# Performance work log

Measured on AMD Instinct MI355X. Metric: run time of the kernel, lower is better.

The kernel has to match this reference:

```python
import jax, jax.numpy as jnp
import numpy as np

NUM_SRC = 100000
NUM_DST = 50000
E = 1200000
IN_FEATS = 128
H = 4
D = 16


def setup_inputs() -> dict:
    key = jax.random.key(0)
    ks = jax.random.split(key, 8)
    feat = jax.random.normal(ks[0], (NUM_DST + NUM_SRC, IN_FEATS), dtype=jnp.float32)
    edge_src = jax.random.randint(ks[1], (E,), 0, NUM_SRC)
    edge_dst = jax.random.randint(ks[2], (E,), 0, NUM_DST)
    # parameters (xavier-normal-ish scale)
    W = jax.random.normal(ks[3], (H * D, IN_FEATS), dtype=jnp.float32) * (2.0 / np.sqrt(IN_FEATS + H * D))
    attn_l = jax.random.normal(ks[4], (H, D), dtype=jnp.float32) * (2.0 / np.sqrt(1 + D))
    attn_r = jax.random.normal(ks[5], (H, D), dtype=jnp.float32) * (2.0 / np.sqrt(1 + D))
    bias = jnp.zeros((H * D,), dtype=jnp.float32)
    return {"feat": feat, "W": W, "attn_l": attn_l, "attn_r": attn_r,
            "bias": bias, "edge_src": edge_src, "edge_dst": edge_dst, "num_dst": NUM_DST}


def reference(feat, W, attn_l, attn_r, bias, edge_src, edge_dst, num_dst):
    negative_slope = 0.2
    n_heads, d_out = attn_l.shape
    # fc: [N, in] @ [in, H*D] -> [N, H, D]
    proj = (feat @ W.T).reshape(feat.shape[0], n_heads, d_out)
    feat_dst = proj[:num_dst]      # [num_dst, H, D]
    feat_src = proj[num_dst:]      # [num_src, H, D]
    el = jnp.einsum('nhd,hd->nh', feat_src, attn_l)  # [num_src, H]
    er = jnp.einsum('nhd,hd->nh', feat_dst, attn_r)  # [num_dst, H]
    # per-edge attention logits (u_add_v + leaky_relu)
    e = jax.nn.leaky_relu(el[edge_src] + er[edge_dst], negative_slope)  # [E, H]
    # segment softmax over destination neighborhoods
    m = jax.ops.segment_max(e, edge_dst, num_segments=num_dst)  # [num_dst, H]
    m = jnp.where(jnp.isfinite(m), m, 0.0)
    e_exp = jnp.exp(e - m[edge_dst])
    denom = jax.ops.segment_sum(e_exp, edge_dst, num_segments=num_dst)  # [num_dst, H]
    a = e_exp / denom[edge_dst]  # [E, H]
    # u_mul_e + sum scatter-aggregate
    msg = feat_src[edge_src] * a[:, :, None]  # [E, H, D]
    rst = jax.ops.segment_sum(msg, edge_dst, num_segments=num_dst)  # [num_dst, H, D]
    rst = rst + bias.reshape(1, n_heads, d_out)
    return rst
```

## Files before the change

### kernel.cpp

```cpp
#include <hip/hip_runtime.h>
#include <hip/hip_bf16.h>


#define NEG_SLOPE 0.2f
#define BSHIFT 7
#define BMASK  127
#define MAXBUK 512
#define FSH    12
#define FCAP   4096
#define EB     2048
#define TILES  4

typedef __attribute__((ext_vector_type(8))) short bf16x8;
typedef __attribute__((ext_vector_type(4))) float f32x4;

__device__ __forceinline__ short f2bf(float f) {
    unsigned u = __float_as_uint(f);
    unsigned r = (u + 0x7fffu + ((u >> 16) & 1u)) >> 16;
    return (short)r;
}
__device__ __forceinline__ unsigned pk2(float a, float b) {
    return (unsigned)(unsigned short)f2bf(a) | ((unsigned)(unsigned short)f2bf(b) << 16);
}

__global__ __launch_bounds__(256) void k_init(const float* __restrict__ W,
                                              short* __restrict__ Wb, int nW,
                                              int* __restrict__ bukcnt) {
    for (int i = threadIdx.x; i < nW; i += 256) Wb[i] = f2bf(W[i]);
    for (int i = threadIdx.x; i < MAXBUK; i += 256) bukcnt[i] = 0;
}

__global__ __launch_bounds__(256) void k_proj_bin(
        const float* __restrict__ feat, const short* __restrict__ Wb,
        const float* __restrict__ attn_l, const float* __restrict__ attn_r,
        unsigned short* __restrict__ projb, float* __restrict__ el, float* __restrict__ er,
        int num_tot, int num_dst, int binB,
        const int* __restrict__ es, const int* __restrict__ ed,
        int* __restrict__ bukcnt, unsigned* __restrict__ pairs, int E, int nbuk) {
    __shared__ __align__(16) char smem_[33792];
    if ((int)blockIdx.x >= binB) {
        unsigned short* fs = (unsigned short*)smem_;
        float* fsf = (float*)(smem_ + 16384);
        const int tid = threadIdx.x;
        const int pb = (int)blockIdx.x - binB;

        const int lane = tid & 63;
        const int wv = tid >> 6;
        const int lr = lane & 15;
        const int lg = lane >> 4;

        float4 pf[8];
        int st_row[4], st_col[4];
#pragma unroll
        for (int it = 0; it < 4; it++) {
            int flat = it * 2048 + tid * 8;
            st_row[it] = flat >> 7;
            st_col[it] = flat & 127;
        }

        auto issue = [&](int t) {
            int nb = pb * (TILES * 64) + t * 64;
#pragma unroll
            for (int it = 0; it < 4; it++) {
                int grow = nb + st_row[it];
                if (grow >= num_tot) grow = num_tot - 1;
                const float4* src = (const float4*)(feat + (size_t)grow * 128 + st_col[it]);
                pf[it * 2] = src[0];
                pf[it * 2 + 1] = src[1];
            }
        };
        auto commit = [&]() {
#pragma unroll
            for (int it = 0; it < 4; it++) {
                float4 x = pf[it * 2], y = pf[it * 2 + 1];
                bf16x8 t;
                t[0] = f2bf(x.x); t[1] = f2bf(x.y); t[2] = f2bf(x.z); t[3] = f2bf(x.w);
                t[4] = f2bf(y.x); t[5] = f2bf(y.y); t[6] = f2bf(y.z); t[7] = f2bf(y.w);
                int slot = st_col[it] >> 3;
                int row = st_row[it];
                *(bf16x8*)&fs[row * 128 + ((slot ^ (row & 15)) << 3)] = t;
            }
        };

        issue(0);
        commit();

        for (int t = 0; t < TILES; t++) {
            __syncthreads();

            bf16x8 afrag[4];
#pragma unroll
            for (int c = 0; c < 4; c++)
                afrag[c] = *(const bf16x8*)&fs[(wv * 16 + lr) * 128 + (((c * 4 + lg) ^ lr) << 3)];

            if (t + 1 < TILES) issue(t + 1);

            f32x4 acc[4];
#pragma unroll
            for (int hh = 0; hh < 4; hh++) acc[hh] = f32x4{0.f, 0.f, 0.f, 0.f};
#pragma unroll
            for (int hh = 0; hh < 4; hh++) {
                const short* bp = Wb + (hh * 16 + lr) * 128 + lg * 8;
#pragma unroll
                for (int c = 0; c < 4; c++) {
                    bf16x8 b = *(const bf16x8*)(bp + c * 32);
                    acc[hh] = __builtin_amdgcn_mfma_f32_16x16x32_bf16(afrag[c], b, acc[hh], 0, 0, 0);
                }
            }

#pragma unroll
            for (int hh = 0; hh < 4; hh++)
#pragma unroll
                for (int r = 0; r < 4; r++)
                    fsf[(wv * 16 + lg * 4 + r) * 68 + hh * 16 + lr] = acc[hh][r];
            __syncthreads();

            {
                int row = tid >> 2, seg = tid & 3;
                int n = pb * (TILES * 64) + t * 64 + row;
                if (n < num_tot) {
                    const float4* rp = (const float4*)&fsf[row * 68 + seg * 16];
                    float4 v0 = rp[0], v1 = rp[1], v2 = rp[2], v3 = rp[3];
                    bool is_dst = n < num_dst;
                    const float* attn = is_dst ? attn_r : attn_l;
                    const float4* ap = (const float4*)&attn[seg * 16];
                    float4 a0 = ap[0], a1 = ap[1], a2 = ap[2], a3 = ap[3];
                    float e = v0.x * a0.x + v0.y * a0.y + v0.z * a0.z + v0.w * a0.w
                            + v1.x * a1.x + v1.y * a1.y + v1.z * a1.z + v1.w * a1.w
                            + v2.x * a2.x + v2.y * a2.y + v2.z * a2.z + v2.w * a2.w
                            + v3.x * a3.x + v3.y * a3.y + v3.z * a3.z + v3.w * a3.w;
                    if (is_dst) {
                        er[(size_t)n * 4 + seg] = e;
                    } else {
                        int sN = n - num_dst;
                        el[(size_t)sN * 4 + seg] = e;
                        uint4 q0, q1;
                        q0.x = pk2(v0.x, v0.y); q0.y = pk2(v0.z, v0.w);
                        q0.z = pk2(v1.x, v1.y); q0.w = pk2(v1.z, v1.w);
                        q1.x = pk2(v2.x, v2.y); q1.y = pk2(v2.z, v2.w);
                        q1.z = pk2(v3.x, v3.y); q1.w = pk2(v3.z, v3.w);
                        uint4* dst = (uint4*)(projb + (size_t)sN * 64 + seg * 16);
                        dst[0] = q0; dst[1] = q1;
                    }
                }
            }

            if (t + 1 < TILES) commit();
        }
    } else {
        int* h = (int*)smem_;
        int* cur = (int*)(smem_ + 2048);
        const int tid = threadIdx.x;
        for (int i = tid; i < MAXBUK; i += 256) h[i] = 0;
        __syncthreads();
        int base = (int)blockIdx.x * EB;
        int rd[8], rs[8];
        if (base + EB <= E) {
            const int4* edp = (const int4*)(ed + base + tid * 8);
            const int4* esp = (const int4*)(es + base + tid * 8);
            int4 d0 = edp[0], d1 = edp[1];
            int4 s0 = esp[0], s1 = esp[1];
            rd[0] = d0.x; rd[1] = d0.y; rd[2] = d0.z; rd[3] = d0.w;
            rd[4] = d1.x; rd[5] = d1.y; rd[6] = d1.z; rd[7] = d1.w;
            rs[0] = s0.x; rs[1] = s0.y; rs[2] = s0.z; rs[3] = s0.w;
            rs[4] = s1.x; rs[5] = s1.y; rs[6] = s1.z; rs[7] = s1.w;
#pragma unroll
            for (int i = 0; i < 8; i++) atomicAdd(&h[rd[i] >> BSHIFT], 1);
        } else {
#pragma unroll
            for (int i = 0; i < 8; i++) {
                int idx = base + tid * 8 + i;
                if (idx < E) {
                    rd[i] = ed[idx];
                    rs[i] = es[idx];
                    atomicAdd(&h[rd[i] >> BSHIFT], 1);
                } else {
                    rd[i] = -1;
                }
            }
        }
        __syncthreads();
        for (int i = tid; i < nbuk; i += 256)
            cur[i] = h[i] ? ((i << FSH) + atomicAdd(&bukcnt[i], h[i])) : 0;
        __syncthreads();
#pragma unroll
        for (int i = 0; i < 8; i++) {
            if (rd[i] >= 0) {
                int d = rd[i];
                int bk = d >> BSHIFT;
                int pos = atomicAdd(&cur[bk], 1);
                if (pos < ((bk + 1) << FSH))
                    pairs[pos] = (unsigned)rs[i] | ((unsigned)(d & BMASK) << 25);
            }
        }
    }
}

__global__ __launch_bounds__(256) void k_fillb(unsigned* __restrict__ pairs,
                                               const int* __restrict__ bukcnt,
                                               int* __restrict__ offs,
                                               int* __restrict__ counts, int nd) {
    __shared__ unsigned lp[FCAP];
    __shared__ int h[128], ex[128], cur[128];
    int b = blockIdx.x;
    int s = b << FSH;
    int cnt = bukcnt[b];
    if (cnt > FCAP) cnt = FCAP;
    if (threadIdx.x < 128) h[threadIdx.x] = 0;
    __syncthreads();
    for (int i = threadIdx.x; i < cnt; i += 256) {
        unsigned v = pairs[s + i];
        lp[i] = v;
        atomicAdd(&h[v >> 25], 1);
    }
    __syncthreads();
    if (threadIdx.x < 128) ex[threadIdx.x] = h[threadIdx.x];
    __syncthreads();
    for (int off = 1; off < 128; off <<= 1) {
        int v = (threadIdx.x >= off && threadIdx.x < 128) ? ex[threadIdx.x - off] : 0;
        __syncthreads();
        if (threadIdx.x < 128) ex[threadIdx.x] += v;
        __syncthreads();
    }
    if (threadIdx.x < 128) {
        int e = ex[threadIdx.x] - h[threadIdx.x];
        cur[threadIdx.x] = e;
        int d = (b << BSHIFT) + threadIdx.x;
        if (d < nd) { offs[d] = s + e; counts[d] = h[threadIdx.x]; }
    }
    __syncthreads();
    for (int i = threadIdx.x; i < cnt; i += 256) {
        unsigned v = lp[i];
        int r = atomicAdd(&cur[v >> 25], 1);
        pairs[s + r] = v & 0x1FFFFFFu;
    }
}

__global__ __launch_bounds__(256) void k_agg(
        const unsigned* __restrict__ csr_src, const int* __restrict__ offs,
        const int* __restrict__ counts, const float* __restrict__ el,
        const float* __restrict__ er, const unsigned short* __restrict__ projb,
        const float* __restrict__ bias, float* __restrict__ out, int nd) {
    int wave = (blockIdx.x * 256 + threadIdx.x) >> 6;
    int lane = threadIdx.x & 63;
    if (wave >= nd) return;
    int d = wave;
    int j = lane & 15, h = lane >> 4;
    int q = lane >> 4, cq = lane & 15;
    int hsrc = (cq >> 2) << 4;
    int start = offs[d], deg = counts[d];
    float er_h = er[d * 4 + h];

    float den = 0.f, a0 = 0.f, a1 = 0.f, a2 = 0.f, a3 = 0.f;
    for (int base = 0; base < deg; base += 16) {
        int cend = deg - base;
        if (cend > 16) cend = 16;
        int sidx = 0;
        float w = 0.f;
        if (j < cend) {
            sidx = (int)csr_src[start + base + j];
            float t = el[sidx * 4 + h] + er_h;
            t = t > 0.f ? t : NEG_SLOPE * t;
            w = __expf(fminf(t, 60.f));
        }
        den += w;
        if (cend == 16) {
#pragma unroll
            for (int t4 = 0; t4 < 4; t4++) {
                int e = 4 * t4 + q;
                int s2 = __shfl(sidx, e);
                float w2 = __shfl(w, hsrc | e);
                uint2 pv = *(const uint2*)(projb + (size_t)s2 * 64 + cq * 4);
                a0 += w2 * __uint_as_float(pv.x << 16);
                a1 += w2 * __uint_as_float(pv.x & 0xffff0000u);
                a2 += w2 * __uint_as_float(pv.y << 16);
                a3 += w2 * __uint_as_float(pv.y & 0xffff0000u);
            }
        } else {
            int steps = (cend + 3) >> 2;
            for (int t4 = 0; t4 < steps; t4++) {
                int e = 4 * t4 + q;
                int s2 = __shfl(sidx, e & 15);
                float w2 = __shfl(w, hsrc | (e & 15));
                uint2 pv = *(const uint2*)(projb + (size_t)s2 * 64 + cq * 4);
                a0 += w2 * __uint_as_float(pv.x << 16);
                a1 += w2 * __uint_as_float(pv.x & 0xffff0000u);
                a2 += w2 * __uint_as_float(pv.y << 16);
                a3 += w2 * __uint_as_float(pv.y & 0xffff0000u);
            }
        }
    }

    den += __shfl_xor(den, 1);
    den += __shfl_xor(den, 2);
    den += __shfl_xor(den, 4);
    den += __shfl_xor(den, 8);
    float den_h = __shfl(den, hsrc);

    a0 += __shfl_xor(a0, 16); a0 += __shfl_xor(a0, 32);
    a1 += __shfl_xor(a1, 16); a1 += __shfl_xor(a1, 32);
    a2 += __shfl_xor(a2, 16); a2 += __shfl_xor(a2, 32);
    a3 += __shfl_xor(a3, 16); a3 += __shfl_xor(a3, 32);

    if (q == 0) {
        float rden = den_h > 0.f ? 1.f / den_h : 0.f;
        float4 o;
        o.x = a0 * rden + bias[cq * 4];
        o.y = a1 * rden + bias[cq * 4 + 1];
        o.z = a2 * rden + bias[cq * 4 + 2];
        o.w = a3 * rden + bias[cq * 4 + 3];
        *(float4*)&out[(size_t)d * 64 + cq * 4] = o;
    }
}

extern "C" void kernel_launch(void* const* d_in, const int* in_sizes, int n_in,
                              void* d_out, int out_size, void* d_ws, size_t ws_size,
                              hipStream_t stream) {
    const float* feat   = (const float*)d_in[0];
    const float* W      = (const float*)d_in[1];
    const float* attn_l = (const float*)d_in[2];
    const float* attn_r = (const float*)d_in[3];
    const float* bias   = (const float*)d_in[4];
    const int*   es     = (const int*)d_in[5];
    const int*   ed     = (const int*)d_in[6];

    const int HD      = in_sizes[2];
    const int in_f    = in_sizes[1] / HD;
    const int num_dst = out_size / HD;
    const int num_tot = in_sizes[0] / in_f;
    const int num_src = num_tot - num_dst;
    const int E       = in_sizes[5];

    float* out = (float*)d_out;

    const int NBUK = (num_dst + BMASK) >> BSHIFT;

    unsigned short* projb = (unsigned short*)d_ws;
    float*    el       = (float*)(projb + (size_t)num_src * 64);
    float*    er       = el + (size_t)num_src * 4;
    int*      counts   = (int*)(er + (size_t)num_dst * 4);
    int*      offs     = counts + num_dst;
    int*      bukcnt   = offs + num_dst;
    unsigned* pairs    = (unsigned*)(bukcnt + MAXBUK);
    short*    Wb       = (short*)(pairs + ((size_t)NBUK << FSH));

    const int projB = (num_tot + TILES * 64 - 1) / (TILES * 64);
    const int binB  = (E + EB - 1) / EB;

    k_init<<<1, 256, 0, stream>>>(W, Wb, HD * in_f, bukcnt);

    k_proj_bin<<<binB + projB, 256, 0, stream>>>(
        feat, Wb, attn_l, attn_r, projb, el, er, num_tot, num_dst, binB,
        es, ed, bukcnt, pairs, E, NBUK);

    k_fillb<<<NBUK, 256, 0, stream>>>(pairs, bukcnt, offs, counts, num_dst);

    k_agg<<<(num_dst * 64 + 255) / 256, 256, 0, stream>>>(
        pairs, offs, counts, el, er, projb, bias, out, num_dst);
}
```

Measured before the change: 102.3 us.

## Fuse bucket CSR fill and attention aggregation into one kernel using LDS

Merges the per-bucket counting sort and the per-destination softmax aggregation into a single 1024-thread kernel per bucket. The sorted source indices stay in shared memory instead of being written back to global memory with offs/counts and re-read. This removes a launch and global traffic, but leaves only one block per bucket (a few hundred blocks of 16 waves each), which reduces parallelism and serializes the sort before aggregation in each block.

```diff
diff --git a/kernel.cpp b/kernel.cpp
--- a/kernel.cpp
+++ b/kernel.cpp
@@ -196,120 +196,124 @@
     }
 }
 
-__global__ __launch_bounds__(256) void k_fillb(unsigned* __restrict__ pairs,
-                                               const int* __restrict__ bukcnt,
-                                               int* __restrict__ offs,
-                                               int* __restrict__ counts, int nd) {
-    __shared__ unsigned lp[FCAP];
+__global__ __launch_bounds__(1024) void k_fagg(
+        const unsigned* __restrict__ pairs, const int* __restrict__ bukcnt,
+        const float* __restrict__ el, const float* __restrict__ er,
+        const unsigned short* __restrict__ projb, const float* __restrict__ bias,
+        float* __restrict__ out, int nd) {
+    __shared__ unsigned lpr[FCAP];
+    __shared__ unsigned lps[FCAP];
     __shared__ int h[128], ex[128], cur[128];
-    int b = blockIdx.x;
-    int s = b << FSH;
+    __shared__ float er_s[128 * 4];
+    const int tid = threadIdx.x;
+    const int b = blockIdx.x;
+    const int dbase = b << BSHIFT;
     int cnt = bukcnt[b];
     if (cnt > FCAP) cnt = FCAP;
-    if (threadIdx.x < 128) h[threadIdx.x] = 0;
-    __syncthreads();
-    for (int i = threadIdx.x; i < cnt; i += 256) {
+    const size_t s = (size_t)b << FSH;
+
+    if (tid < 128) h[tid] = 0;
+    if (tid < 512) {
+        int d = dbase + (tid >> 2);
+        er_s[tid] = (d < nd) ? er[(size_t)d * 4 + (tid & 3)] : 0.f;
+    }
+    __syncthreads();
+    for (int i = tid; i < cnt; i += 1024) {
         unsigned v = pairs[s + i];
-        lp[i] = v;
+        lpr[i] = v;
         atomicAdd(&h[v >> 25], 1);
     }
     __syncthreads();
-    if (threadIdx.x < 128) ex[threadIdx.x] = h[threadIdx.x];
+    if (tid < 128) ex[tid] = h[tid];
     __syncthreads();
     for (int off = 1; off < 128; off <<= 1) {
-        int v = (threadIdx.x >= off && threadIdx.x < 128) ? ex[threadIdx.x - off] : 0;
-        __syncthreads();
-        if (threadIdx.x < 128) ex[threadIdx.x] += v;
-        __syncthreads();
-    }
-    if (threadIdx.x < 128) {
-        int e = ex[threadIdx.x] - h[threadIdx.x];
-        cur[threadIdx.x] = e;
-        int d = (b << BSHIFT) + threadIdx.x;
-        if (d < nd) { offs[d] = s + e; counts[d] = h[threadIdx.x]; }
-    }
-    __syncthreads();
-    for (int i = threadIdx.x; i < cnt; i += 256) {
-        unsigned v = lp[i];
+        int v = (tid >= off && tid < 128) ? ex[tid - off] : 0;
+        __syncthreads();
+        if (tid < 128) ex[tid] += v;
+        __syncthreads();
+    }
+    if (tid < 128) cur[tid] = ex[tid] - h[tid];
+    __syncthreads();
+    for (int i = tid; i < cnt; i += 1024) {
+        unsigned v = lpr[i];
         int r = atomicAdd(&cur[v >> 25], 1);
-        pairs[s + r] = v & 0x1FFFFFFu;
-    }
-}
-
-__global__ __launch_bounds__(256) void k_agg(
-        const unsigned* __restrict__ csr_src, const int* __restrict__ offs,
-        const int* __restrict__ counts, const float* __restrict__ el,
-        const float* __restrict__ er, const unsigned short* __restrict__ projb,
-        const float* __restrict__ bias, float* __restrict__ out, int nd) {
-    int wave = (blockIdx.x * 256 + threadIdx.x) >> 6;
-    int lane = threadIdx.x & 63;
-    if (wave >= nd) return;
-    int d = wave;
-    int j = lane & 15, h = lane >> 4;
+        lps[r] = v & 0x1FFFFFFu;
+    }
+    __syncthreads();
+
+    const int lane = tid & 63;
+    const int wid = tid >> 6;
+    int j = lane & 15, hh = lane >> 4;
     int q = lane >> 4, cq = lane & 15;
     int hsrc = (cq >> 2) << 4;
-    int start = offs[d], deg = counts[d];
-    float er_h = er[d * 4 + h];
-
-    float den = 0.f, a0 = 0.f, a1 = 0.f, a2 = 0.f, a3 = 0.f;
-    for (int base = 0; base < deg; base += 16) {
-        int cend = deg - base;
-        if (cend > 16) cend = 16;
-        int sidx = 0;
-        float w = 0.f;
-        if (j < cend) {
-            sidx = (int)csr_src[start + base + j];
-            float t = el[sidx * 4 + h] + er_h;
-            t = t > 0.f ? t : NEG_SLOPE * t;
-            w = __expf(fminf(t, 60.f));
-        }
-        den += w;
-        if (cend == 16) {
-#pragma unroll
-            for (int t4 = 0; t4 < 4; t4++) {
-                int e = 4 * t4 + q;
-                int s2 = __shfl(sidx, e);
-                float w2 = __shfl(w, hsrc | e);
-                uint2 pv = *(const uint2*)(projb + (size_t)s2 * 64 + cq * 4);
-                a0 += w2 * __uint_as_float(pv.x << 16);
-                a1 += w2 * __uint_as_float(pv.x & 0xffff0000u);
-                a2 += w2 * __uint_as_float(pv.y << 16);
-                a3 += w2 * __uint_as_float(pv.y & 0xffff0000u);
-            }
-        } else {
-            int steps = (cend + 3) >> 2;
-            for (int t4 = 0; t4 < steps; t4++) {
-                int e = 4 * t4 + q;
-                int s2 = __shfl(sidx, e & 15);
-                float w2 = __shfl(w, hsrc | (e & 15));
-                uint2 pv = *(const uint2*)(projb + (size_t)s2 * 64 + cq * 4);
-                a0 += w2 * __uint_as_float(pv.x << 16);
-                a1 += w2 * __uint_as_float(pv.x & 0xffff0000u);
-                a2 += w2 * __uint_as_float(pv.y << 16);
-                a3 += w2 * __uint_as_float(pv.y & 0xffff0000u);
-            }
-        }
-    }
-
-    den += __shfl_xor(den, 1);
-    den += __shfl_xor(den, 2);
-    den += __shfl_xor(den, 4);
-    den += __shfl_xor(den, 8);
-    float den_h = __shfl(den, hsrc);
-
-    a0 += __shfl_xor(a0, 16); a0 += __shfl_xor(a0, 32);
-    a1 += __shfl_xor(a1, 16); a1 += __shfl_xor(a1, 32);
-    a2 += __shfl_xor(a2, 16); a2 += __shfl_xor(a2, 32);
-    a3 += __shfl_xor(a3, 16); a3 += __shfl_xor(a3, 32);
-
-    if (q == 0) {
-        float rden = den_h > 0.f ? 1.f / den_h : 0.f;
-        float4 o;
-        o.x = a0 * rden + bias[cq * 4];
-        o.y = a1 * rden + bias[cq * 4 + 1];
-        o.z = a2 * rden + bias[cq * 4 + 2];
-        o.w = a3 * rden + bias[cq * 4 + 3];
-        *(float4*)&out[(size_t)d * 64 + cq * 4] = o;
+
+    for (int dl = wid; dl < 128; dl += 16) {
+        int d = dbase + dl;
+        if (d >= nd) break;
+        int deg = h[dl];
+        int start = ex[dl] - deg;
+        float er_h = er_s[dl * 4 + hh];
+
+        float den = 0.f, a0 = 0.f, a1 = 0.f, a2 = 0.f, a3 = 0.f;
+        for (int base = 0; base < deg; base += 16) {
+            int cend = deg - base;
+            if (cend > 16) cend = 16;
+            int sidx = 0;
+            float w = 0.f;
+            if (j < cend) {
+                sidx = (int)lps[start + base + j];
+                float t = el[sidx * 4 + hh] + er_h;
+                t = t > 0.f ? t : NEG_SLOPE * t;
+                w = __expf(fminf(t, 60.f));
+            }
+            den += w;
+            if (cend == 16) {
+#pragma unroll
+                for (int t4 = 0; t4 < 4; t4++) {
+                    int e = 4 * t4 + q;
+                    int s2 = __shfl(sidx, e);
+                    float w2 = __shfl(w, hsrc | e);
+                    uint2 pv = *(const uint2*)(projb + (size_t)s2 * 64 + cq * 4);
+                    a0 += w2 * __uint_as_float(pv.x << 16);
+                    a1 += w2 * __uint_as_float(pv.x & 0xffff0000u);
+                    a2 += w2 * __uint_as_float(pv.y << 16);
+                    a3 += w2 * __uint_as_float(pv.y & 0xffff0000u);
+                }
+            } else {
+                int steps = (cend + 3) >> 2;
+                for (int t4 = 0; t4 < steps; t4++) {
+                    int e = 4 * t4 + q;
+                    int s2 = __shfl(sidx, e & 15);
+                    float w2 = __shfl(w, hsrc | (e & 15));
+                    uint2 pv = *(const uint2*)(projb + (size_t)s2 * 64 + cq * 4);
+                    a0 += w2 * __uint_as_float(pv.x << 16);
+                    a1 += w2 * __uint_as_float(pv.x & 0xffff0000u);
+                    a2 += w2 * __uint_as_float(pv.y << 16);
+                    a3 += w2 * __uint_as_float(pv.y & 0xffff0000u);
+                }
+            }
+        }
+
+        den += __shfl_xor(den, 1);
+        den += __shfl_xor(den, 2);
+        den += __shfl_xor(den, 4);
+        den += __shfl_xor(den, 8);
+        float den_h = __shfl(den, hsrc);
+
+        a0 += __shfl_xor(a0, 16); a0 += __shfl_xor(a0, 32);
+        a1 += __shfl_xor(a1, 16); a1 += __shfl_xor(a1, 32);
+        a2 += __shfl_xor(a2, 16); a2 += __shfl_xor(a2, 32);
+        a3 += __shfl_xor(a3, 16); a3 += __shfl_xor(a3, 32);
+
+        if (q == 0) {
+            float rden = den_h > 0.f ? 1.f / den_h : 0.f;
+            float4 o;
+            o.x = a0 * rden + bias[cq * 4];
+            o.y = a1 * rden + bias[cq * 4 + 1];
+            o.z = a2 * rden + bias[cq * 4 + 2];
+            o.w = a3 * rden + bias[cq * 4 + 3];
+            *(float4*)&out[(size_t)d * 64 + cq * 4] = o;
+        }
     }
 }
 
@@ -338,9 +342,7 @@
     unsigned short* projb = (unsigned short*)d_ws;
     float*    el       = (float*)(projb + (size_t)num_src * 64);
     float*    er       = el + (size_t)num_src * 4;
-    int*      counts   = (int*)(er + (size_t)num_dst * 4);
-    int*      offs     = counts + num_dst;
-    int*      bukcnt   = offs + num_dst;
+    int*      bukcnt   = (int*)(er + (size_t)num_dst * 4);
     unsigned* pairs    = (unsigned*)(bukcnt + MAXBUK);
     short*    Wb       = (short*)(pairs + ((size_t)NBUK << FSH));
 
@@ -353,8 +355,6 @@
         feat, Wb, attn_l, attn_r, projb, el, er, num_tot, num_dst, binB,
         es, ed, bukcnt, pairs, E, NBUK);
 
-    k_fillb<<<NBUK, 256, 0, stream>>>(pairs, bukcnt, offs, counts, num_dst);
-
-    k_agg<<<(num_dst * 64 + 255) / 256, 256, 0, stream>>>(
-        pairs, offs, counts, el, er, projb, bias, out, num_dst);
-}
+    k_fagg<<<NBUK, 1024, 0, stream>>>(
+        pairs, bukcnt, el, er, projb, bias, out, num_dst);
+}
```

Measured after the change: 112.3 us. 1.1x slower.
